# Kernel optimization log

Hardware: AMD Instinct MI355X
Metric: run time of the kernel (lower is better)

Reference implementation:

```python
import jax, jax.numpy as jnp
import numpy as np

N = 50000
E = 800000
D = 128  # input_dim = hidden_dim = output_dim
N_LAYERS = 3


def _graph_conv(x, src, dst, edge_weight, w_rel, b_rel, w_root):
    # PyG GraphConv (aggr='add'):
    #   out = lin_rel( sum_{j in N(i)} edge_weight_ij * x_j ) + lin_root(x_i)
    msg = x[src] * edge_weight[:, None]                      # [E, D_in]
    agg = jax.ops.segment_sum(msg, dst, num_segments=x.shape[0])  # [N, D_in]
    return agg @ w_rel + b_rel + x @ w_root                  # [N, D_out]


def setup_inputs() -> dict:
    key = jax.random.key(0)
    ks = jax.random.split(key, 4 + 3 * N_LAYERS)
    x = jax.random.normal(ks[0], (N, D), dtype=jnp.float32)
    edge_index = jax.random.randint(ks[1], (2, E), 0, N, dtype=jnp.int32)
    edge_attr = jax.random.uniform(ks[2], (E,), dtype=jnp.float32)
    scale = 1.0 / np.sqrt(D)
    inp = {"x": x, "edge_index": edge_index, "edge_attr": edge_attr}
    for l in range(N_LAYERS):
        inp[f"w_rel{l}"] = jax.random.normal(ks[3 + 3 * l], (D, D), dtype=jnp.float32) * scale
        inp[f"b_rel{l}"] = jnp.zeros((D,), dtype=jnp.float32)
        inp[f"w_root{l}"] = jax.random.normal(ks[4 + 3 * l], (D, D), dtype=jnp.float32) * scale
    return inp


def reference(x, edge_index, edge_attr,
              w_rel0, b_rel0, w_root0,
              w_rel1, b_rel1, w_root1,
              w_rel2, b_rel2, w_root2):
    src, dst = edge_index[0], edge_index[1]
    params = [(w_rel0, b_rel0, w_root0), (w_rel1, b_rel1, w_root1), (w_rel2, b_rel2, w_root2)]
    h = x
    for w_rel, b_rel, w_root in params[:-1]:
        h = _graph_conv(h, src, dst, edge_attr, w_rel, b_rel, w_root)
        h = jax.nn.relu(h)  # dropout p=0.0 -> identity
    w_rel, b_rel, w_root = params[-1]
    return _graph_conv(h, src, dst, edge_attr, w_rel, b_rel, w_root)
```

## Files before the change

### kernel.cpp

```cpp
#include <hip/hip_runtime.h>
#include <hip/hip_bf16.h>
#include <hip/hip_fp16.h>

#define N_NODES 50000
#define N_EDGES 800000
#define DIM 128

#define NBUCK 391
#define BCAP  2816
#define CHUNK 2048

#define CVT_BLOCKS 25000

#define LDSROW 136

typedef float floatx4 __attribute__((ext_vector_type(4)));
typedef float floatx2 __attribute__((ext_vector_type(2)));
typedef short shortx8 __attribute__((ext_vector_type(8)));

__device__ __forceinline__ unsigned short f2bf(float f) {
    union { float f; unsigned int u; } c; c.f = f;
    unsigned int u = c.u;
    unsigned int r = (u + 0x7FFFu + ((u >> 16) & 1u)) >> 16;
    return (unsigned short)r;
}
__device__ __forceinline__ floatx2 bf2x2(unsigned int p) {
    union { unsigned int u; float f; } lo, hi;
    lo.u = p << 16; hi.u = p & 0xFFFF0000u;
    return (floatx2){lo.f, hi.f};
}

__global__ __launch_bounds__(256)
void prep_kernel(const float* __restrict__ x, unsigned short* __restrict__ X,
                 const float* __restrict__ wr0, const float* __restrict__ wt0,
                 const float* __restrict__ wr1, const float* __restrict__ wt1,
                 const float* __restrict__ wr2, const float* __restrict__ wt2,
                 unsigned short* __restrict__ Wp, int* __restrict__ bcursor) {
    int b = blockIdx.x;
    if (b < CVT_BLOCKS) {
        int i = b * 256 + threadIdx.x;
        X[i] = f2bf(x[i]);
    } else if (b == CVT_BLOCKS) {
        for (int i = threadIdx.x; i < NBUCK; i += 256) bcursor[i] = 0;
    } else {
        int id = (b - CVT_BLOCKS - 1) * 256 + threadIdx.x;
        int layer = id >> 15;
        int rem = id & 32767;
        int j  = rem & 7;
        int L  = (rem >> 3) & 63;
        int ct = (rem >> 9) & 7;
        int t  = rem >> 12;
        int k = t * 32 + (L >> 4) * 8 + j;
        int c = ct * 16 + (L & 15);
        const float* wr = (layer == 0) ? wr0 : (layer == 1) ? wr1 : wr2;
        const float* wt = (layer == 0) ? wt0 : (layer == 1) ? wt1 : wt2;
        float v = (k < 128) ? wr[k * 128 + c] : wt[(k - 128) * 128 + c];
        Wp[id] = f2bf(v);
    }
}

__global__ __launch_bounds__(512)
void partition_kernel(const int* __restrict__ src, const int* __restrict__ dst,
                      const float* __restrict__ ew,
                      int* __restrict__ bcursor, int2* __restrict__ bstage, int e) {
    __shared__ int2 stage[CHUNK];
    __shared__ int cnt[NBUCK];
    __shared__ int lbase[NBUCK];
    __shared__ int gbase[NBUCK];
    __shared__ int wsum[8];
    const int tid = threadIdx.x;
    const int e0 = blockIdx.x * CHUNK;
    const int ecnt = min(CHUNK, e - e0);

    for (int i = tid; i < NBUCK; i += 512) cnt[i] = 0;
    __syncthreads();
    for (int i = tid; i < ecnt; i += 512)
        atomicAdd(&cnt[dst[e0 + i] >> 7], 1);
    __syncthreads();

    {
        int v = (tid < NBUCK) ? cnt[tid] : 0;
        int lane = tid & 63, wid = tid >> 6;
        int acc = v;
#pragma unroll
        for (int off = 1; off < 64; off <<= 1) {
            int t = __shfl_up(acc, off, 64);
            if (lane >= off) acc += t;
        }
        if (lane == 63) wsum[wid] = acc;
        __syncthreads();
        int wpref = 0;
        for (int w = 0; w < wid; ++w) wpref += wsum[w];
        int excl = wpref + acc - v;
        if (tid < NBUCK) {
            lbase[tid] = excl;
            gbase[tid] = atomicAdd(&bcursor[tid], v);
            cnt[tid] = 0;
        }
    }
    __syncthreads();

    for (int i = tid; i < ecnt; i += 512) {
        int d = dst[e0 + i];
        int s = src[e0 + i];
        unsigned int hw = (unsigned int)__half_as_ushort(__float2half(ew[e0 + i]));
        int b = d >> 7;
        int pos = atomicAdd(&cnt[b], 1);
        stage[lbase[b] + pos] = make_int2((int)((hw << 16) | (unsigned int)s), d);
    }
    __syncthreads();

    for (int j = tid; j < ecnt; j += 512) {
        int2 p = stage[j];
        int b = p.y >> 7;
        int gidx = b * BCAP + gbase[b] + (j - lbase[b]);
        bstage[gidx] = p;
    }
}

__global__ __launch_bounds__(256)
void bucket_fill_kernel(const int2* __restrict__ bstage, const int* __restrict__ bcursor,
                        int* __restrict__ row_start, unsigned int* __restrict__ perm4, int n) {
    __shared__ int cnt128[128];
    __shared__ int curs[128];
    __shared__ int wsum[4];
    __shared__ int sbase, scnt;
    const int tid = threadIdx.x;
    const int b = blockIdx.x;
    const int node0 = b << 7;
    const int lane = tid & 63, wid = tid >> 6;

    {
        int i0 = tid * 2, i1 = tid * 2 + 1;
        int v0 = (i0 < NBUCK) ? bcursor[i0] : 0;
        int v1 = (i1 < NBUCK) ? bcursor[i1] : 0;
        int s = v0 + v1;
        int acc = s;
#pragma unroll
        for (int off = 1; off < 64; off <<= 1) {
            int t = __shfl_up(acc, off, 64);
            if (lane >= off) acc += t;
        }
        if (lane == 63) wsum[wid] = acc;
        __syncthreads();
        int wpref = 0;
        for (int w = 0; w < wid; ++w) wpref += wsum[w];
        int excl = wpref + acc - s;
        if (i0 == b) { sbase = excl;      scnt = v0; }
        if (i1 == b) { sbase = excl + v0; scnt = v1; }
    }
    __syncthreads();
    const int cntb = scnt;
    const int base = sbase;
    const int2* sp = bstage + (size_t)b * BCAP;

    if (tid < 128) cnt128[tid] = 0;
    __syncthreads();
    for (int i = tid; i < cntb; i += 256)
        atomicAdd(&cnt128[sp[i].y & 127], 1);
    __syncthreads();

    int v = (tid < 128) ? cnt128[tid] : 0;
    int acc = v;
#pragma unroll
    for (int off = 1; off < 64; off <<= 1) {
        int t = __shfl_up(acc, off, 64);
        if (lane >= off) acc += t;
    }
    if (lane == 63) wsum[wid] = acc;
    __syncthreads();
    int wpref = 0;
    for (int w = 0; w < wid; ++w) wpref += wsum[w];
    int excl = wpref + acc - v;
    if (tid < 128) {
        int node = node0 + tid;
        if (node <= n) row_start[node] = base + excl;
        curs[tid] = excl;
    }
    __syncthreads();

    for (int i = tid; i < cntb; i += 256) {
        int2 p = sp[i];
        int pos = atomicAdd(&curs[p.y & 127], 1);
        perm4[base + pos] = (unsigned int)p.x;
    }
}

__global__ __launch_bounds__(256, 8)
void fused_layer(const unsigned short* __restrict__ h, const int* __restrict__ row_start,
                 const unsigned int* __restrict__ perm4, const unsigned short* __restrict__ Wp,
                 const float* __restrict__ bias, float* __restrict__ outF,
                 unsigned short* __restrict__ outB, int n, int relu) {
    __shared__ unsigned short Gs[16 * LDSROW];
    const int tid  = threadIdx.x;
    const int lane = tid & 63;
    const int wid  = tid >> 6;
    const int g  = lane >> 4;
    const int sl = lane & 15;
    const int rowT = blockIdx.x * 16;
    const int nodeBase = rowT + wid * 4;

    int rs = 0;
    if (lane < 5) {
        int idx = nodeBase + lane;
        rs = row_start[idx <= n ? idx : n];
    }

    for (int nd = 0; nd < 4; ++nd) {
        if (nodeBase + nd >= n) break;
        int beg = __shfl(rs, nd, 64);
        int end = __shfl(rs, nd + 1, 64);
        floatx2 ac[4];
#pragma unroll
        for (int k = 0; k < 4; ++k) ac[k] = (floatx2){0.f, 0.f};
        for (int t = beg; t < end; t += 16) {
            int i0 = t + g, i1 = t + 4 + g, i2 = t + 8 + g, i3 = t + 12 + g;
            unsigned int p0 = (i0 < end) ? perm4[i0] : 0;
            unsigned int p1 = (i1 < end) ? perm4[i1] : 0;
            unsigned int p2 = (i2 < end) ? perm4[i2] : 0;
            unsigned int p3 = (i3 < end) ? perm4[i3] : 0;
            int s0 = p0 & 0xFFFF, s1 = p1 & 0xFFFF, s2 = p2 & 0xFFFF, s3 = p3 & 0xFFFF;
            uint4 v0 = *(const uint4*)(h + (size_t)s0 * DIM + sl * 8);
            uint4 v1 = *(const uint4*)(h + (size_t)s1 * DIM + sl * 8);
            uint4 v2 = *(const uint4*)(h + (size_t)s2 * DIM + sl * 8);
            uint4 v3 = *(const uint4*)(h + (size_t)s3 * DIM + sl * 8);
            float w0 = __half2float(__ushort_as_half((unsigned short)(p0 >> 16)));
            float w1 = __half2float(__ushort_as_half((unsigned short)(p1 >> 16)));
            float w2 = __half2float(__ushort_as_half((unsigned short)(p2 >> 16)));
            float w3 = __half2float(__ushort_as_half((unsigned short)(p3 >> 16)));
            floatx2 W0 = (floatx2){w0, w0}, W1 = (floatx2){w1, w1};
            floatx2 W2 = (floatx2){w2, w2}, W3 = (floatx2){w3, w3};
            ac[0] += W0 * bf2x2(v0.x); ac[1] += W0 * bf2x2(v0.y);
            ac[2] += W0 * bf2x2(v0.z); ac[3] += W0 * bf2x2(v0.w);
            ac[0] += W1 * bf2x2(v1.x); ac[1] += W1 * bf2x2(v1.y);
            ac[2] += W1 * bf2x2(v1.z); ac[3] += W1 * bf2x2(v1.w);
            ac[0] += W2 * bf2x2(v2.x); ac[1] += W2 * bf2x2(v2.y);
            ac[2] += W2 * bf2x2(v2.z); ac[3] += W2 * bf2x2(v2.w);
            ac[0] += W3 * bf2x2(v3.x); ac[1] += W3 * bf2x2(v3.y);
            ac[2] += W3 * bf2x2(v3.z); ac[3] += W3 * bf2x2(v3.w);
        }
        float acc[8] = {ac[0].x, ac[0].y, ac[1].x, ac[1].y,
                        ac[2].x, ac[2].y, ac[3].x, ac[3].y};
#pragma unroll
        for (int k = 0; k < 8; ++k) {
            acc[k] += __shfl_xor(acc[k], 16, 64);
            acc[k] += __shfl_xor(acc[k], 32, 64);
        }
        if (lane < 16) {
            uint4 r;
            r.x = (unsigned int)f2bf(acc[0]) | ((unsigned int)f2bf(acc[1]) << 16);
            r.y = (unsigned int)f2bf(acc[2]) | ((unsigned int)f2bf(acc[3]) << 16);
            r.z = (unsigned int)f2bf(acc[4]) | ((unsigned int)f2bf(acc[5]) << 16);
            r.w = (unsigned int)f2bf(acc[6]) | ((unsigned int)f2bf(acc[7]) << 16);
            *(uint4*)(&Gs[(wid * 4 + nd) * LDSROW + sl * 8]) = r;
        }
    }
    __syncthreads();

    floatx4 acc2[2];
#pragma unroll
    for (int ct = 0; ct < 2; ++ct) acc2[ct] = (floatx4){0.f, 0.f, 0.f, 0.f};

    int rGlob = rowT + sl;
    int rr = (rGlob < n) ? rGlob : (n - 1);
    const int ko = g * 8;
#pragma unroll
    for (int t = 0; t < 8; ++t) {
        shortx8 a;
        if (t < 4)
            a = *(const shortx8*)(&Gs[sl * LDSROW + t * 32 + ko]);
        else
            a = *(const shortx8*)(h + (size_t)rr * DIM + (t - 4) * 32 + ko);
        const unsigned short* wp = Wp + (size_t)t * 4096 + (wid * 2) * 512 + lane * 8;
#pragma unroll
        for (int ct = 0; ct < 2; ++ct) {
            shortx8 b = *(const shortx8*)(wp + ct * 512);
            acc2[ct] = __builtin_amdgcn_mfma_f32_16x16x32_bf16(a, b, acc2[ct], 0, 0, 0);
        }
    }

#pragma unroll
    for (int ct = 0; ct < 2; ++ct) {
        int col = wid * 32 + ct * 16 + sl;
        float bv = bias[col];
#pragma unroll
        for (int i = 0; i < 4; ++i) {
            int row = rowT + g * 4 + i;
            if (row < n) {
                float v = acc2[ct][i] + bv;
                if (relu) v = fmaxf(v, 0.f);
                if (outF) outF[(size_t)row * DIM + col] = v;
                else      outB[(size_t)row * DIM + col] = f2bf(v);
            }
        }
    }
}

extern "C" void kernel_launch(void* const* d_in, const int* in_sizes, int n_in,
                              void* d_out, int out_size, void* d_ws, size_t ws_size,
                              hipStream_t stream) {
    const int N = N_NODES, E = N_EDGES;

    const float* x   = (const float*)d_in[0];
    const int*   ei  = (const int*)d_in[1];
    const float* ea  = (const float*)d_in[2];
    const float* wr0 = (const float*)d_in[3];
    const float* br0 = (const float*)d_in[4];
    const float* wt0 = (const float*)d_in[5];
    const float* wr1 = (const float*)d_in[6];
    const float* br1 = (const float*)d_in[7];
    const float* wt1 = (const float*)d_in[8];
    const float* wr2 = (const float*)d_in[9];
    const float* br2 = (const float*)d_in[10];
    const float* wt2 = (const float*)d_in[11];
    const int* srcI = ei;
    const int* dstI = ei + E;
    float* out = (float*)d_out;

    int2* bstage = (int2*)d_ws;
    unsigned short* X  = (unsigned short*)(bstage + (size_t)NBUCK * BCAP);
    unsigned short* H1 = X + (size_t)N * DIM;
    unsigned short* H2 = H1 + (size_t)N * DIM;
    unsigned short* Wp = H2 + (size_t)N * DIM;
    unsigned int* perm4 = (unsigned int*)(Wp + 3 * 32768);
    int* bcursor = (int*)(perm4 + E);
    int* rowst   = bcursor + NBUCK;

    prep_kernel<<<CVT_BLOCKS + 1 + 384, 256, 0, stream>>>(x, X, wr0, wt0, wr1, wt1, wr2, wt2, Wp, bcursor);
    partition_kernel<<<(E + CHUNK - 1) / CHUNK, 512, 0, stream>>>(srcI, dstI, ea, bcursor, bstage, E);
    bucket_fill_kernel<<<NBUCK, 256, 0, stream>>>(bstage, bcursor, rowst, perm4, N);

    const int fusedGrid = (N + 15) / 16;

    fused_layer<<<fusedGrid, 256, 0, stream>>>(X,  rowst, perm4, Wp,         br0, nullptr, H1, N, 1);
    fused_layer<<<fusedGrid, 256, 0, stream>>>(H1, rowst, perm4, Wp + 32768, br1, nullptr, H2, N, 1);
    fused_layer<<<fusedGrid, 256, 0, stream>>>(H2, rowst, perm4, Wp + 65536, br2, out, nullptr, N, 0);
}
```

Baseline: 245.8 us.

## Bucket edges per 16-node tile and fold CSR fill into first layer

Edges are now partitioned into 3125 buckets of 16 destination nodes each, matching the fused layer's 16-row tile, so the separate bucket_fill kernel goes away. The first fused_layer sorts its bucket's edges by node in LDS and writes a compact per-tile row-start and permutation for later layers to reuse, and each layer stages its edge list in LDS before the gather. This removes one launch and a global CSR pass, and the partition kernel now keeps edges in registers instead of rereading them. The cost is a fixed per-bucket capacity of 384 edges, which overflows if any 16-node group gets more in-degree, plus larger LDS arrays in the partition kernel.

Result: slower. 280.9 us (+14.3%).

```diff
diff --git a/kernel.cpp b/kernel.cpp
--- a/kernel.cpp
+++ b/kernel.cpp
@@ -6,8 +6,9 @@
 #define N_EDGES 800000
 #define DIM 128
 
-#define NBUCK 391
-#define BCAP  2816
+#define NBUCK 3125
+#define BCAPW 384
+#define NPAD  3328
 #define CHUNK 2048
 
 #define CVT_BLOCKS 25000
@@ -59,29 +60,45 @@
     }
 }
 
-__global__ __launch_bounds__(512)
+__global__ __launch_bounds__(256)
 void partition_kernel(const int* __restrict__ src, const int* __restrict__ dst,
                       const float* __restrict__ ew,
                       int* __restrict__ bcursor, int2* __restrict__ bstage, int e) {
     __shared__ int2 stage[CHUNK];
-    __shared__ int cnt[NBUCK];
-    __shared__ int lbase[NBUCK];
-    __shared__ int gbase[NBUCK];
-    __shared__ int wsum[8];
+    __shared__ int cnt[NPAD];
+    __shared__ int lbase[NPAD];
+    __shared__ int gbase[NPAD];
+    __shared__ int wsum[4];
     const int tid = threadIdx.x;
+    const int lane = tid & 63, wid = tid >> 6;
     const int e0 = blockIdx.x * CHUNK;
     const int ecnt = min(CHUNK, e - e0);
 
-    for (int i = tid; i < NBUCK; i += 512) cnt[i] = 0;
-    __syncthreads();
-    for (int i = tid; i < ecnt; i += 512)
-        atomicAdd(&cnt[dst[e0 + i] >> 7], 1);
+    for (int i = tid; i < NPAD; i += 256) cnt[i] = 0;
+    __syncthreads();
+
+    int2 ep[8]; int eb[8];
+    int ne = 0;
+    for (int k = 0; k < 8; ++k) {
+        int i = tid + k * 256;
+        if (i < ecnt) {
+            int d = dst[e0 + i];
+            int s = src[e0 + i];
+            unsigned int hw = (unsigned int)__half_as_ushort(__float2half(ew[e0 + i]));
+            ep[k] = make_int2((int)((hw << 16) | (unsigned int)s), d);
+            eb[k] = d >> 4;
+            atomicAdd(&cnt[eb[k]], 1);
+            ne = k + 1;
+        }
+    }
     __syncthreads();
 
     {
-        int v = (tid < NBUCK) ? cnt[tid] : 0;
-        int lane = tid & 63, wid = tid >> 6;
-        int acc = v;
+        int loc[13];
+        int s = 0;
+#pragma unroll
+        for (int j = 0; j < 13; ++j) { loc[j] = cnt[tid * 13 + j]; s += loc[j]; }
+        int acc = s;
 #pragma unroll
         for (int off = 1; off < 64; off <<= 1) {
             int t = __shfl_up(acc, off, 64);
@@ -91,134 +108,113 @@
         __syncthreads();
         int wpref = 0;
         for (int w = 0; w < wid; ++w) wpref += wsum[w];
-        int excl = wpref + acc - v;
-        if (tid < NBUCK) {
-            lbase[tid] = excl;
-            gbase[tid] = atomicAdd(&bcursor[tid], v);
-            cnt[tid] = 0;
-        }
-    }
-    __syncthreads();
-
-    for (int i = tid; i < ecnt; i += 512) {
-        int d = dst[e0 + i];
-        int s = src[e0 + i];
-        unsigned int hw = (unsigned int)__half_as_ushort(__float2half(ew[e0 + i]));
-        int b = d >> 7;
+        int run = wpref + acc - s;
+#pragma unroll
+        for (int j = 0; j < 13; ++j) {
+            int b = tid * 13 + j;
+            lbase[b] = run;
+            int c = loc[j];
+            if (c > 0 && b < NBUCK) gbase[b] = atomicAdd(&bcursor[b], c);
+            run += c;
+            cnt[b] = 0;
+        }
+    }
+    __syncthreads();
+
+    for (int k = 0; k < ne; ++k) {
+        int b = eb[k];
         int pos = atomicAdd(&cnt[b], 1);
-        stage[lbase[b] + pos] = make_int2((int)((hw << 16) | (unsigned int)s), d);
-    }
-    __syncthreads();
-
-    for (int j = tid; j < ecnt; j += 512) {
+        stage[lbase[b] + pos] = ep[k];
+    }
+    __syncthreads();
+
+    for (int j = tid; j < ecnt; j += 256) {
         int2 p = stage[j];
-        int b = p.y >> 7;
-        int gidx = b * BCAP + gbase[b] + (j - lbase[b]);
+        int b = p.y >> 4;
+        int gidx = b * BCAPW + gbase[b] + (j - lbase[b]);
         bstage[gidx] = p;
     }
 }
 
-__global__ __launch_bounds__(256)
-void bucket_fill_kernel(const int2* __restrict__ bstage, const int* __restrict__ bcursor,
-                        int* __restrict__ row_start, unsigned int* __restrict__ perm4, int n) {
-    __shared__ int cnt128[128];
-    __shared__ int curs[128];
-    __shared__ int wsum[4];
-    __shared__ int sbase, scnt;
-    const int tid = threadIdx.x;
-    const int b = blockIdx.x;
-    const int node0 = b << 7;
-    const int lane = tid & 63, wid = tid >> 6;
-
-    {
-        int i0 = tid * 2, i1 = tid * 2 + 1;
-        int v0 = (i0 < NBUCK) ? bcursor[i0] : 0;
-        int v1 = (i1 < NBUCK) ? bcursor[i1] : 0;
-        int s = v0 + v1;
-        int acc = s;
-#pragma unroll
-        for (int off = 1; off < 64; off <<= 1) {
-            int t = __shfl_up(acc, off, 64);
-            if (lane >= off) acc += t;
-        }
-        if (lane == 63) wsum[wid] = acc;
-        __syncthreads();
-        int wpref = 0;
-        for (int w = 0; w < wid; ++w) wpref += wsum[w];
-        int excl = wpref + acc - s;
-        if (i0 == b) { sbase = excl;      scnt = v0; }
-        if (i1 == b) { sbase = excl + v0; scnt = v1; }
-    }
-    __syncthreads();
-    const int cntb = scnt;
-    const int base = sbase;
-    const int2* sp = bstage + (size_t)b * BCAP;
-
-    if (tid < 128) cnt128[tid] = 0;
-    __syncthreads();
-    for (int i = tid; i < cntb; i += 256)
-        atomicAdd(&cnt128[sp[i].y & 127], 1);
-    __syncthreads();
-
-    int v = (tid < 128) ? cnt128[tid] : 0;
-    int acc = v;
-#pragma unroll
-    for (int off = 1; off < 64; off <<= 1) {
-        int t = __shfl_up(acc, off, 64);
-        if (lane >= off) acc += t;
-    }
-    if (lane == 63) wsum[wid] = acc;
-    __syncthreads();
-    int wpref = 0;
-    for (int w = 0; w < wid; ++w) wpref += wsum[w];
-    int excl = wpref + acc - v;
-    if (tid < 128) {
-        int node = node0 + tid;
-        if (node <= n) row_start[node] = base + excl;
-        curs[tid] = excl;
-    }
-    __syncthreads();
-
-    for (int i = tid; i < cntb; i += 256) {
-        int2 p = sp[i];
-        int pos = atomicAdd(&curs[p.y & 127], 1);
-        perm4[base + pos] = (unsigned int)p.x;
-    }
-}
-
 __global__ __launch_bounds__(256, 8)
-void fused_layer(const unsigned short* __restrict__ h, const int* __restrict__ row_start,
-                 const unsigned int* __restrict__ perm4, const unsigned short* __restrict__ Wp,
-                 const float* __restrict__ bias, float* __restrict__ outF,
-                 unsigned short* __restrict__ outB, int n, int relu) {
+void fused_layer(const unsigned short* __restrict__ h,
+                 const int2* __restrict__ bstage, const int* __restrict__ bcursor,
+                 const int* __restrict__ rowst17, const unsigned int* __restrict__ perm4,
+                 int* __restrict__ w_rowst17, unsigned int* __restrict__ w_perm4,
+                 const unsigned short* __restrict__ Wp, const float* __restrict__ bias,
+                 float* __restrict__ outF, unsigned short* __restrict__ outB,
+                 int n, int relu, int fill) {
     __shared__ unsigned short Gs[16 * LDSROW];
+    __shared__ unsigned int win4[BCAPW];
+    __shared__ int excl17[17];
+    __shared__ int cnt16[16];
     const int tid  = threadIdx.x;
     const int lane = tid & 63;
     const int wid  = tid >> 6;
     const int g  = lane >> 4;
     const int sl = lane & 15;
-    const int rowT = blockIdx.x * 16;
-    const int nodeBase = rowT + wid * 4;
-
-    int rs = 0;
-    if (lane < 5) {
-        int idx = nodeBase + lane;
-        rs = row_start[idx <= n ? idx : n];
-    }
-
+    const int b = blockIdx.x;
+    const int rowT = b * 16;
+
+    if (fill) {
+        const int cntb = bcursor[b];
+        if (tid < 16) cnt16[tid] = 0;
+        __syncthreads();
+        unsigned int pay[2]; int nod[2]; int nh = 0;
+#pragma unroll
+        for (int k = 0; k < 2; ++k) {
+            int i = tid + k * 256;
+            if (i < cntb) {
+                int2 p = bstage[b * BCAPW + i];
+                pay[k] = (unsigned int)p.x;
+                nod[k] = p.y & 15;
+                atomicAdd(&cnt16[nod[k]], 1);
+                nh = k + 1;
+            }
+        }
+        __syncthreads();
+        if (tid < 64) {
+            int v = (lane < 16) ? cnt16[lane] : 0;
+            int acc = v;
+#pragma unroll
+            for (int off = 1; off < 16; off <<= 1) {
+                int t = __shfl_up(acc, off, 64);
+                if (lane >= off) acc += t;
+            }
+            if (lane < 16) { excl17[lane] = acc - v; cnt16[lane] = acc - v; }
+            if (lane == 15) excl17[16] = acc;
+        }
+        __syncthreads();
+        for (int k = 0; k < nh; ++k) {
+            int pos = atomicAdd(&cnt16[nod[k]], 1);
+            win4[pos] = pay[k];
+        }
+        if (tid < 17) w_rowst17[b * 17 + tid] = excl17[tid];
+        __syncthreads();
+        for (int i = tid; i < excl17[16]; i += 256)
+            w_perm4[b * BCAPW + i] = win4[i];
+    } else {
+        if (tid < 17) excl17[tid] = rowst17[b * 17 + tid];
+        __syncthreads();
+        const int cntb = excl17[16];
+        for (int i = tid; i < cntb; i += 256)
+            win4[i] = perm4[b * BCAPW + i];
+        __syncthreads();
+    }
+
+    const int ndBase = wid * 4;
     for (int nd = 0; nd < 4; ++nd) {
-        if (nodeBase + nd >= n) break;
-        int beg = __shfl(rs, nd, 64);
-        int end = __shfl(rs, nd + 1, 64);
+        int beg = excl17[ndBase + nd];
+        int end = excl17[ndBase + nd + 1];
         floatx2 ac[4];
 #pragma unroll
         for (int k = 0; k < 4; ++k) ac[k] = (floatx2){0.f, 0.f};
         for (int t = beg; t < end; t += 16) {
             int i0 = t + g, i1 = t + 4 + g, i2 = t + 8 + g, i3 = t + 12 + g;
-            unsigned int p0 = (i0 < end) ? perm4[i0] : 0;
-            unsigned int p1 = (i1 < end) ? perm4[i1] : 0;
-            unsigned int p2 = (i2 < end) ? perm4[i2] : 0;
-            unsigned int p3 = (i3 < end) ? perm4[i3] : 0;
+            unsigned int p0 = (i0 < end) ? win4[i0] : 0;
+            unsigned int p1 = (i1 < end) ? win4[i1] : 0;
+            unsigned int p2 = (i2 < end) ? win4[i2] : 0;
+            unsigned int p3 = (i3 < end) ? win4[i3] : 0;
             int s0 = p0 & 0xFFFF, s1 = p1 & 0xFFFF, s2 = p2 & 0xFFFF, s3 = p3 & 0xFFFF;
             uint4 v0 = *(const uint4*)(h + (size_t)s0 * DIM + sl * 8);
             uint4 v1 = *(const uint4*)(h + (size_t)s1 * DIM + sl * 8);
@@ -252,7 +248,7 @@
             r.y = (unsigned int)f2bf(acc[2]) | ((unsigned int)f2bf(acc[3]) << 16);
             r.z = (unsigned int)f2bf(acc[4]) | ((unsigned int)f2bf(acc[5]) << 16);
             r.w = (unsigned int)f2bf(acc[6]) | ((unsigned int)f2bf(acc[7]) << 16);
-            *(uint4*)(&Gs[(wid * 4 + nd) * LDSROW + sl * 8]) = r;
+            *(uint4*)(&Gs[(ndBase + nd) * LDSROW + sl * 8]) = r;
         }
     }
     __syncthreads();
@@ -274,8 +270,8 @@
         const unsigned short* wp = Wp + (size_t)t * 4096 + (wid * 2) * 512 + lane * 8;
 #pragma unroll
         for (int ct = 0; ct < 2; ++ct) {
-            shortx8 b = *(const shortx8*)(wp + ct * 512);
-            acc2[ct] = __builtin_amdgcn_mfma_f32_16x16x32_bf16(a, b, acc2[ct], 0, 0, 0);
+            shortx8 b2 = *(const shortx8*)(wp + ct * 512);
+            acc2[ct] = __builtin_amdgcn_mfma_f32_16x16x32_bf16(a, b2, acc2[ct], 0, 0, 0);
         }
     }
 
@@ -318,21 +314,21 @@
     float* out = (float*)d_out;
 
     int2* bstage = (int2*)d_ws;
-    unsigned short* X  = (unsigned short*)(bstage + (size_t)NBUCK * BCAP);
+    unsigned short* X  = (unsigned short*)(bstage + (size_t)NBUCK * BCAPW);
     unsigned short* H1 = X + (size_t)N * DIM;
     unsigned short* H2 = H1 + (size_t)N * DIM;
     unsigned short* Wp = H2 + (size_t)N * DIM;
     unsigned int* perm4 = (unsigned int*)(Wp + 3 * 32768);
-    int* bcursor = (int*)(perm4 + E);
-    int* rowst   = bcursor + NBUCK;
+    int* bcursor = (int*)(perm4 + (size_t)NBUCK * BCAPW);
+    int* rowst17 = bcursor + NBUCK;
 
     prep_kernel<<<CVT_BLOCKS + 1 + 384, 256, 0, stream>>>(x, X, wr0, wt0, wr1, wt1, wr2, wt2, Wp, bcursor);
-    partition_kernel<<<(E + CHUNK - 1) / CHUNK, 512, 0, stream>>>(srcI, dstI, ea, bcursor, bstage, E);
-    bucket_fill_kernel<<<NBUCK, 256, 0, stream>>>(bstage, bcursor, rowst, perm4, N);
-
-    const int fusedGrid = (N + 15) / 16;
-
-    fused_layer<<<fusedGrid, 256, 0, stream>>>(X,  rowst, perm4, Wp,         br0, nullptr, H1, N, 1);
-    fused_layer<<<fusedGrid, 256, 0, stream>>>(H1, rowst, perm4, Wp + 32768, br1, nullptr, H2, N, 1);
-    fused_layer<<<fusedGrid, 256, 0, stream>>>(H2, rowst, perm4, Wp + 65536, br2, out, nullptr, N, 0);
-}
+    partition_kernel<<<(E + CHUNK - 1) / CHUNK, 256, 0, stream>>>(srcI, dstI, ea, bcursor, bstage, E);
+
+    fused_layer<<<NBUCK, 256, 0, stream>>>(X,  bstage, bcursor, rowst17, perm4, rowst17, perm4,
+                                           Wp,         br0, nullptr, H1, N, 1, 1);
+    fused_layer<<<NBUCK, 256, 0, stream>>>(H1, bstage, bcursor, rowst17, perm4, rowst17, perm4,
+                                           Wp + 32768, br1, nullptr, H2, N, 1, 0);
+    fused_layer<<<NBUCK, 256, 0, stream>>>(H2, bstage, bcursor, rowst17, perm4, rowst17, perm4,
+                                           Wp + 65536, br2, out, nullptr, N, 0, 0);
+}
```
